# Optimization experiments

Hardware: AMD Instinct MI355X
Metric: run time of the kernel (lower is better)

The kernel has to match this reference:

```python
import jax, jax.numpy as jnp
import numpy as np

B, C, H, W = 2, 512, 48, 48
HEADS, DHEAD = 8, 64
INNER = HEADS * DHEAD  # 512
CTX_LEN, CTX_DIM = 77, 768
FF_INNER = 4 * INNER   # 2048 (GEGLU inner dim)
GN_GROUPS, GN_EPS, LN_EPS = 32, 1e-6, 1e-5
SCALE = DHEAD ** -0.5


def setup_inputs() -> dict:
    key = jax.random.key(0)
    ks = iter(jax.random.split(key, 32))
    def nrm(shape, s=0.02):
        return jax.random.normal(next(ks), shape, jnp.float32) * s
    return dict(
        x=jax.random.normal(next(ks), (B, C, H, W), jnp.float32),
        context=jax.random.normal(next(ks), (B, CTX_LEN, CTX_DIM), jnp.float32),
        gn_g=jnp.ones((C,), jnp.float32), gn_b=jnp.zeros((C,), jnp.float32),
        w_in=nrm((C, INNER)), b_in=jnp.zeros((INNER,), jnp.float32),
        ln1_g=jnp.ones((INNER,), jnp.float32), ln1_b=jnp.zeros((INNER,), jnp.float32),
        wq1=nrm((INNER, INNER)), wk1=nrm((INNER, INNER)), wv1=nrm((INNER, INNER)),
        wo1=nrm((INNER, INNER)), bo1=jnp.zeros((INNER,), jnp.float32),
        ln2_g=jnp.ones((INNER,), jnp.float32), ln2_b=jnp.zeros((INNER,), jnp.float32),
        wq2=nrm((INNER, INNER)), wk2=nrm((CTX_DIM, INNER)), wv2=nrm((CTX_DIM, INNER)),
        wo2=nrm((INNER, INNER)), bo2=jnp.zeros((INNER,), jnp.float32),
        ln3_g=jnp.ones((INNER,), jnp.float32), ln3_b=jnp.zeros((INNER,), jnp.float32),
        w_ff1=nrm((INNER, 2 * FF_INNER)), b_ff1=jnp.zeros((2 * FF_INNER,), jnp.float32),
        w_ff2=nrm((FF_INNER, INNER)), b_ff2=jnp.zeros((INNER,), jnp.float32),
        w_out=nrm((INNER, C)), b_out=jnp.zeros((C,), jnp.float32),
    )


def _layernorm(x, g, b):
    m = jnp.mean(x, -1, keepdims=True)
    v = jnp.var(x, -1, keepdims=True)
    return (x - m) * jax.lax.rsqrt(v + LN_EPS) * g + b


def _groupnorm(x, g, b):
    bs, c, h, w = x.shape
    xg = x.reshape(bs, GN_GROUPS, c // GN_GROUPS, h, w)
    m = jnp.mean(xg, (2, 3, 4), keepdims=True)
    v = jnp.var(xg, (2, 3, 4), keepdims=True)
    xg = (xg - m) * jax.lax.rsqrt(v + GN_EPS)
    return xg.reshape(bs, c, h, w) * g[None, :, None, None] + b[None, :, None, None]


def _attn(x, ctx, wq, wk, wv, wo, bo):
    bs, n, _ = x.shape
    m = ctx.shape[1]
    q = (x @ wq).reshape(bs, n, HEADS, DHEAD).transpose(0, 2, 1, 3)    # b h n d
    k = (ctx @ wk).reshape(bs, m, HEADS, DHEAD).transpose(0, 2, 1, 3)  # b h m d
    v = (ctx @ wv).reshape(bs, m, HEADS, DHEAD).transpose(0, 2, 1, 3)
    sim = jnp.einsum('bhid,bhjd->bhij', q, k) * SCALE
    a = jax.nn.softmax(sim, axis=-1)
    o = jnp.einsum('bhij,bhjd->bhid', a, v)
    o = o.transpose(0, 2, 1, 3).reshape(bs, n, INNER)
    return o @ wo + bo


def reference(x, context, gn_g, gn_b, w_in, b_in,
              ln1_g, ln1_b, wq1, wk1, wv1, wo1, bo1,
              ln2_g, ln2_b, wq2, wk2, wv2, wo2, bo2,
              ln3_g, ln3_b, w_ff1, b_ff1, w_ff2, b_ff2,
              w_out, b_out):
    x_in = x
    h = _groupnorm(x, gn_g, gn_b)
    # proj_in: 1x1 conv == channel-wise linear
    h = jnp.einsum('bchw,cd->bdhw', h, w_in) + b_in[None, :, None, None]
    t = h.reshape(B, INNER, H * W).transpose(0, 2, 1)  # b n c
    # BasicTransformerBlock (depth=1)
    hn = _layernorm(t, ln1_g, ln1_b)
    t = _attn(hn, hn, wq1, wk1, wv1, wo1, bo1) + t          # self-attention
    hn = _layernorm(t, ln2_g, ln2_b)
    t = _attn(hn, context, wq2, wk2, wv2, wo2, bo2) + t     # cross-attention
    hn = _layernorm(t, ln3_g, ln3_b)
    u = hn @ w_ff1 + b_ff1                                   # GEGLU proj
    a_, g_ = jnp.split(u, 2, axis=-1)
    t = (a_ * jax.nn.gelu(g_, approximate=False)) @ w_ff2 + b_ff2 + t
    # back to image + proj_out 1x1 conv + residual
    y = t.transpose(0, 2, 1).reshape(B, INNER, H, W)
    y = jnp.einsum('bchw,cd->bdhw', y, w_out) + b_out[None, :, None, None]
    return y + x_in
```

## Files before the change

kernel.cpp:

```cpp
#include <hip/hip_runtime.h>
#include <hip/hip_bf16.h>

typedef __bf16 bf16_t;
typedef __bf16 bf16x4 __attribute__((ext_vector_type(4)));
typedef __bf16 bf16x8 __attribute__((ext_vector_type(8)));
typedef float f32x4 __attribute__((ext_vector_type(4)));

static __device__ __forceinline__ bf16x8 bzero8() {
  bf16x8 v;
#pragma unroll
  for (int j = 0; j < 8; j++) v[j] = (bf16_t)0.f;
  return v;
}

static __device__ __forceinline__ void async_copy16(const bf16_t* g, bf16_t* l) {
  __builtin_amdgcn_global_load_lds((const __attribute__((address_space(1))) void*)g,
                                   (__attribute__((address_space(3))) void*)l,
                                   16, 0, 0);
}
#define WAVE_LGKM() asm volatile("s_waitcnt lgkmcnt(0)" ::: "memory")

static __device__ __forceinline__ float fast_exp2(float x) {
  float r;
  asm volatile("v_exp_f32 %0, %1" : "=v"(r) : "v"(x));
  return r;
}

#define QK_SCALE 0.18033688f

__global__ void probe_kernel(const void* x, int* flag) {
  if (threadIdx.x != 0 || blockIdx.x != 0) return;
  const unsigned short* u = (const unsigned short*)x;
  int insane = 0;
  for (int j = 0; j < 512; j++) {
    unsigned short h = u[j];
    int e = (h >> 7) & 0xFF;
    if (e == 0xFF || e > 140 || (e != 0 && e < 100)) insane++;
  }
  *flag = (insane > 16) ? 1 : 0;
}

struct ConvArgs { const void* src[28]; int n[28]; int off[28]; };
__global__ __launch_bounds__(256) void convert_kernel(ConvArgs a, const int* flag,
                                                      bf16_t* dst) {
  int i = blockIdx.y;
  if (i >= 28) return;
  int n = a.n[i];
  if (n == 0) return;
  const void* s = a.src[i];
  bf16_t* d = dst + a.off[i];
  bool f32 = (*flag != 0);
  int n4 = n >> 2;
  for (int j = blockIdx.x * 256 + threadIdx.x; j < n4; j += gridDim.x * 256) {
    bf16x4 o;
    if (f32) {
      float4 v = ((const float4*)s)[j];
      o[0] = (bf16_t)v.x; o[1] = (bf16_t)v.y; o[2] = (bf16_t)v.z; o[3] = (bf16_t)v.w;
    } else {
      o = ((const bf16x4*)s)[j];
    }
    ((bf16x4*)d)[j] = o;
  }
  int base = n4 << 2;
  int j = base + blockIdx.x * 256 + threadIdx.x;
  if (j < n) {
    float v = f32 ? ((const float*)s)[j] : (float)((const bf16_t*)s)[j];
    d[j] = (bf16_t)v;
  }
}

struct TransArgs { const void* src[10]; int dst_off[10]; int K[10]; int N[10]; };
__global__ __launch_bounds__(256) void transpose_kernel(TransArgs ta, const int* flag,
                                                        bf16_t* __restrict__ wt) {
  int wi = blockIdx.y;
  int K = ta.K[wi], N = ta.N[wi];
  int tiles_n = N >> 6;
  int tile = blockIdx.x;
  if (tile >= tiles_n * (K >> 6)) return;
  int tk = tile / tiles_n, tn = tile - tk * tiles_n;
  int k0 = tk * 64, n0 = tn * 64;
  bf16_t* dst = wt + ta.dst_off[wi];
  bool f32 = (*flag != 0);
  __shared__ bf16_t tl[64][66];
  int t = threadIdx.x;
  int r = t >> 2, c = (t & 3) * 16;
  if (f32) {
    const float* src = (const float*)ta.src[wi] + (size_t)(k0 + r) * N + n0 + c;
#pragma unroll
    for (int q = 0; q < 4; q++) {
      float4 v = *(const float4*)(src + q * 4);
      tl[r][c + q * 4 + 0] = (bf16_t)v.x;
      tl[r][c + q * 4 + 1] = (bf16_t)v.y;
      tl[r][c + q * 4 + 2] = (bf16_t)v.z;
      tl[r][c + q * 4 + 3] = (bf16_t)v.w;
    }
  } else {
    const bf16_t* src = (const bf16_t*)ta.src[wi] + (size_t)(k0 + r) * N + n0 + c;
    bf16x8 v0 = *(const bf16x8*)(src);
    bf16x8 v1 = *(const bf16x8*)(src + 8);
#pragma unroll
    for (int j = 0; j < 8; j++) { tl[r][c + j] = v0[j]; tl[r][c + 8 + j] = v1[j]; }
  }
  __syncthreads();
  bf16x8 o0, o1;
#pragma unroll
  for (int j = 0; j < 8; j++) { o0[j] = tl[c + j][r]; o1[j] = tl[c + 8 + j][r]; }
  *(bf16x8*)(dst + (size_t)(n0 + r) * K + k0 + c) = o0;
  *(bf16x8*)(dst + (size_t)(n0 + r) * K + k0 + c + 8) = o1;
}

__global__ __launch_bounds__(256) void gn_stats_kernel(const bf16_t* __restrict__ x,
                                                       float* __restrict__ stats) {
  const bf16x8* base = (const bf16x8*)(x + (size_t)blockIdx.x * 36864);
  float s = 0.f, ss = 0.f;
  for (int i = threadIdx.x; i < 4608; i += 256) {
    bf16x8 v = base[i];
#pragma unroll
    for (int j = 0; j < 8; j++) { float f = (float)v[j]; s += f; ss += f * f; }
  }
  __shared__ float red[8];
#pragma unroll
  for (int off = 32; off > 0; off >>= 1) { s += __shfl_down(s, off); ss += __shfl_down(ss, off); }
  int wid = threadIdx.x >> 6;
  if ((threadIdx.x & 63) == 0) { red[wid] = s; red[4 + wid] = ss; }
  __syncthreads();
  if (threadIdx.x == 0) {
    float S = red[0] + red[1] + red[2] + red[3];
    float SS = red[4] + red[5] + red[6] + red[7];
    const float inv = 1.0f / 36864.0f;
    float mean = S * inv;
    float var = SS * inv - mean * mean;
    stats[blockIdx.x * 2] = mean;
    stats[blockIdx.x * 2 + 1] = rsqrtf(fmaxf(var, 0.f) + 1e-6f);
  }
}

__global__ __launch_bounds__(256) void gn_apply_kernel(const bf16_t* __restrict__ x,
                                                       const float* __restrict__ stats,
                                                       const bf16_t* __restrict__ g,
                                                       const bf16_t* __restrict__ bb,
                                                       bf16_t* __restrict__ xnt) {
  int p0 = blockIdx.x * 64, c0 = blockIdx.y * 64, bz = blockIdx.z;
  __shared__ bf16_t tl[64][66];
  int t = threadIdx.x;
  int r = t >> 2, cc = (t & 3) * 16;
  int c = c0 + r;
  float mean = stats[(bz * 32 + (c >> 4)) * 2];
  float rstd = stats[(bz * 32 + (c >> 4)) * 2 + 1];
  float gg = (float)g[c], bbv = (float)bb[c];
  const bf16_t* row = x + ((size_t)(bz * 512 + c)) * 2304 + p0 + cc;
  bf16x8 v0 = *(const bf16x8*)(row);
  bf16x8 v1 = *(const bf16x8*)(row + 8);
#pragma unroll
  for (int j = 0; j < 8; j++) {
    tl[r][cc + j] = (bf16_t)(((float)v0[j] - mean) * rstd * gg + bbv);
    tl[r][cc + 8 + j] = (bf16_t)(((float)v1[j] - mean) * rstd * gg + bbv);
  }
  __syncthreads();
  bf16x8 o0, o1;
#pragma unroll
  for (int j = 0; j < 8; j++) { o0[j] = tl[cc + j][r]; o1[j] = tl[cc + 8 + j][r]; }
  bf16_t* orow = xnt + ((size_t)(bz * 2304 + p0 + r)) * 512 + c0 + cc;
  *(bf16x8*)(orow) = o0;
  *(bf16x8*)(orow + 8) = o1;
}

__global__ __launch_bounds__(256) void ln_kernel(const float* __restrict__ in,
                                                 const bf16_t* __restrict__ g,
                                                 const bf16_t* __restrict__ b,
                                                 bf16_t* __restrict__ out) {
  int tok = blockIdx.x * 4 + (threadIdx.x >> 6);
  int lane = threadIdx.x & 63;
  const float* row = in + (size_t)tok * 512 + lane * 8;
  float f[8];
  float s = 0.f, ss = 0.f;
#pragma unroll
  for (int j = 0; j < 8; j++) { f[j] = row[j]; s += f[j]; ss += f[j] * f[j]; }
#pragma unroll
  for (int off = 32; off > 0; off >>= 1) { s += __shfl_xor(s, off); ss += __shfl_xor(ss, off); }
  float mean = s * (1.0f / 512.0f);
  float var = ss * (1.0f / 512.0f) - mean * mean;
  float rstd = rsqrtf(fmaxf(var, 0.f) + 1e-5f);
  bf16x8 gv = *(const bf16x8*)(g + lane * 8);
  bf16x8 bv = *(const bf16x8*)(b + lane * 8);
  bf16x8 o;
#pragma unroll
  for (int j = 0; j < 8; j++) o[j] = (bf16_t)((f[j] - mean) * rstd * (float)gv[j] + (float)bv[j]);
  *(bf16x8*)(out + (size_t)tok * 512 + lane * 8) = o;
}

template <int SMODE, int MODE>
__global__ __launch_bounds__(256) void gemm64d_kernel(
    const bf16_t* __restrict__ A, int lda,
    const bf16_t* __restrict__ Bt, int K, int N,
    const bf16_t* __restrict__ bias, float oscale,
    float* __restrict__ t32, bf16_t* __restrict__ C,
    const bf16_t* __restrict__ resb, const float* __restrict__ resf,
    float* __restrict__ Cf, const int* dflag) {
  __shared__ bf16_t As[2][4096];
  __shared__ bf16_t Bs[2][4096];
  int t = threadIdx.x, w = t >> 6, quad = (t >> 4) & 3, l16 = t & 15;
  int m0 = blockIdx.y * 64, n0 = blockIdx.x * 64;
  int wm = (w >> 1) * 32, wn = (w & 1) * 32;
  const f32x4 z4 = {0.f, 0.f, 0.f, 0.f};
  f32x4 acc[2][2] = {{z4, z4}, {z4, z4}};
  int r0 = t >> 3, c0 = ((t & 7) ^ (r0 & 7)) * 8;
  int r1 = r0 + 32, c1 = ((t & 7) ^ (r1 & 7)) * 8;
  const bf16_t* Ar0 = A + (size_t)(m0 + r0) * lda + c0;
  const bf16_t* Ar1 = A + (size_t)(m0 + r1) * lda + c1;
  const bf16_t* Br0 = Bt + (size_t)(n0 + r0) * K + c0;
  const bf16_t* Br1 = Bt + (size_t)(n0 + r1) * K + c1;
  int niter = K >> 6;
  async_copy16(Ar0, As[0] + w * 512);
  async_copy16(Ar1, As[0] + 2048 + w * 512);
  async_copy16(Br0, Bs[0] + w * 512);
  async_copy16(Br1, Bs[0] + 2048 + w * 512);
  for (int it = 0; it < niter; it++) {
    __syncthreads();
    if (it + 1 < niter) {
      int k0 = (it + 1) << 6;
      int nb = (it + 1) & 1;
      async_copy16(Ar0 + k0, As[nb] + w * 512);
      async_copy16(Ar1 + k0, As[nb] + 2048 + w * 512);
      async_copy16(Br0 + k0, Bs[nb] + w * 512);
      async_copy16(Br1 + k0, Bs[nb] + 2048 + w * 512);
    }
    int cb = it & 1;
    bf16x8 af[2][2], bff[2][2];
#pragma unroll
    for (int mi = 0; mi < 2; mi++) {
      int rr = wm + mi * 16 + l16;
      af[mi][0] = *(const bf16x8*)&As[cb][(rr * 8 + (quad ^ (rr & 7))) * 8];
      af[mi][1] = *(const bf16x8*)&As[cb][(rr * 8 + ((quad + 4) ^ (rr & 7))) * 8];
    }
#pragma unroll
    for (int ni = 0; ni < 2; ni++) {
      int rr = wn + ni * 16 + l16;
      bff[ni][0] = *(const bf16x8*)&Bs[cb][(rr * 8 + (quad ^ (rr & 7))) * 8];
      bff[ni][1] = *(const bf16x8*)&Bs[cb][(rr * 8 + ((quad + 4) ^ (rr & 7))) * 8];
    }
#pragma unroll
    for (int mi = 0; mi < 2; mi++)
#pragma unroll
      for (int ni = 0; ni < 2; ni++) {
        acc[mi][ni] = __builtin_amdgcn_mfma_f32_16x16x32_bf16(af[mi][0], bff[ni][0], acc[mi][ni], 0, 0, 0);
        acc[mi][ni] = __builtin_amdgcn_mfma_f32_16x16x32_bf16(af[mi][1], bff[ni][1], acc[mi][ni], 0, 0, 0);
      }
  }
  const bool f32m = (MODE == 3) && (*dflag != 0);
#pragma unroll
  for (int mi = 0; mi < 2; mi++)
#pragma unroll
    for (int ni = 0; ni < 2; ni++) {
      int col = n0 + wn + ni * 16 + l16;
      float bv = bias ? (float)bias[col] : 0.f;
#pragma unroll
      for (int r = 0; r < 4; r++) {
        int row = m0 + wm + mi * 16 + quad * 4 + r;
        float v = acc[mi][ni][r] + bv;
        size_t addr;
        if (SMODE == 0) {
          addr = (size_t)row * N + col;
        } else {
          int b2 = row / 2304; int p = row - b2 * 2304;
          addr = ((size_t)(b2 * 512 + col)) * 2304 + p;
        }
        if (MODE == 0) C[addr] = (bf16_t)(v * oscale);
        else if (MODE == 1) { t32[addr] = v; C[addr] = (bf16_t)v; }
        else if (MODE == 2) { v += t32[addr]; t32[addr] = v; C[addr] = (bf16_t)v; }
        else {
          v += f32m ? resf[addr] : (float)resb[addr];
          if (f32m) Cf[addr] = v; else C[addr] = (bf16_t)v;
        }
      }
    }
}

__global__ __launch_bounds__(256) void qkv_kernel(
    const bf16_t* __restrict__ A,
    const bf16_t* __restrict__ BtQ, const bf16_t* __restrict__ BtK,
    const bf16_t* __restrict__ BtV,
    bf16_t* __restrict__ Qo, bf16_t* __restrict__ Ko, bf16_t* __restrict__ Vt) {
  __shared__ bf16_t As[2][4096];
  __shared__ bf16_t Bs[2][4096];
  int z = blockIdx.z;
  const bf16_t* Bt = (z == 0) ? BtQ : (z == 1) ? BtK : BtV;
  int t = threadIdx.x, w = t >> 6, quad = (t >> 4) & 3, l16 = t & 15;
  int m0 = blockIdx.y * 64, n0 = blockIdx.x * 64;
  int wm = (w >> 1) * 32, wn = (w & 1) * 32;
  const f32x4 z4 = {0.f, 0.f, 0.f, 0.f};
  f32x4 acc[2][2] = {{z4, z4}, {z4, z4}};
  int r0 = t >> 3, c0 = ((t & 7) ^ (r0 & 7)) * 8;
  int r1 = r0 + 32, c1 = ((t & 7) ^ (r1 & 7)) * 8;
  const bf16_t* Ar0 = A + (size_t)(m0 + r0) * 512 + c0;
  const bf16_t* Ar1 = A + (size_t)(m0 + r1) * 512 + c1;
  const bf16_t* Br0 = Bt + (size_t)(n0 + r0) * 512 + c0;
  const bf16_t* Br1 = Bt + (size_t)(n0 + r1) * 512 + c1;
  async_copy16(Ar0, As[0] + w * 512);
  async_copy16(Ar1, As[0] + 2048 + w * 512);
  async_copy16(Br0, Bs[0] + w * 512);
  async_copy16(Br1, Bs[0] + 2048 + w * 512);
  for (int it = 0; it < 8; it++) {
    __syncthreads();
    if (it + 1 < 8) {
      int k0 = (it + 1) << 6;
      int nb = (it + 1) & 1;
      async_copy16(Ar0 + k0, As[nb] + w * 512);
      async_copy16(Ar1 + k0, As[nb] + 2048 + w * 512);
      async_copy16(Br0 + k0, Bs[nb] + w * 512);
      async_copy16(Br1 + k0, Bs[nb] + 2048 + w * 512);
    }
    int cb = it & 1;
    bf16x8 af[2][2], bff[2][2];
#pragma unroll
    for (int mi = 0; mi < 2; mi++) {
      int rr = wm + mi * 16 + l16;
      af[mi][0] = *(const bf16x8*)&As[cb][(rr * 8 + (quad ^ (rr & 7))) * 8];
      af[mi][1] = *(const bf16x8*)&As[cb][(rr * 8 + ((quad + 4) ^ (rr & 7))) * 8];
    }
#pragma unroll
    for (int ni = 0; ni < 2; ni++) {
      int rr = wn + ni * 16 + l16;
      bff[ni][0] = *(const bf16x8*)&Bs[cb][(rr * 8 + (quad ^ (rr & 7))) * 8];
      bff[ni][1] = *(const bf16x8*)&Bs[cb][(rr * 8 + ((quad + 4) ^ (rr & 7))) * 8];
    }
#pragma unroll
    for (int mi = 0; mi < 2; mi++)
#pragma unroll
      for (int ni = 0; ni < 2; ni++) {
        acc[mi][ni] = __builtin_amdgcn_mfma_f32_16x16x32_bf16(af[mi][0], bff[ni][0], acc[mi][ni], 0, 0, 0);
        acc[mi][ni] = __builtin_amdgcn_mfma_f32_16x16x32_bf16(af[mi][1], bff[ni][1], acc[mi][ni], 0, 0, 0);
      }
  }
#pragma unroll
  for (int mi = 0; mi < 2; mi++)
#pragma unroll
    for (int ni = 0; ni < 2; ni++) {
      int col = n0 + wn + ni * 16 + l16;
#pragma unroll
      for (int r = 0; r < 4; r++) {
        int row = m0 + wm + mi * 16 + quad * 4 + r;
        float v = acc[mi][ni][r];
        if (z == 0) Qo[(size_t)row * 512 + col] = (bf16_t)(v * QK_SCALE);
        else if (z == 1) Ko[(size_t)row * 512 + col] = (bf16_t)v;
        else {
          int b2 = row / 2304; int p = row - b2 * 2304;
          Vt[((size_t)(b2 * 512 + col)) * 2304 + p] = (bf16_t)v;
        }
      }
    }
}

__global__ __launch_bounds__(256) void ff1_kernel(const bf16_t* __restrict__ A,
                                                  const bf16_t* __restrict__ Bt,
                                                  const bf16_t* __restrict__ bias,
                                                  bf16_t* __restrict__ U) {
  __shared__ bf16_t As[2][4096];
  __shared__ bf16_t Ba[2][4096];
  __shared__ bf16_t Bg[2][4096];
  int t = threadIdx.x, w = t >> 6, quad = (t >> 4) & 3, l16 = t & 15;
  int m0 = blockIdx.y * 64, n0 = blockIdx.x * 64;
  int wm = (w >> 1) * 32, wn = (w & 1) * 32;
  const f32x4 z4 = {0.f, 0.f, 0.f, 0.f};
  f32x4 aa[2][2] = {{z4, z4}, {z4, z4}};
  f32x4 ag[2][2] = {{z4, z4}, {z4, z4}};
  int r0 = t >> 3, c0 = ((t & 7) ^ (r0 & 7)) * 8;
  int r1 = r0 + 32, c1 = ((t & 7) ^ (r1 & 7)) * 8;
  const bf16_t* Ar0 = A + (size_t)(m0 + r0) * 512 + c0;
  const bf16_t* Ar1 = A + (size_t)(m0 + r1) * 512 + c1;
  const bf16_t* Ba0 = Bt + (size_t)(n0 + r0) * 512 + c0;
  const bf16_t* Ba1 = Bt + (size_t)(n0 + r1) * 512 + c1;
  const bf16_t* Bg0 = Bt + (size_t)(2048 + n0 + r0) * 512 + c0;
  const bf16_t* Bg1 = Bt + (size_t)(2048 + n0 + r1) * 512 + c1;
  async_copy16(Ar0, As[0] + w * 512);
  async_copy16(Ar1, As[0] + 2048 + w * 512);
  async_copy16(Ba0, Ba[0] + w * 512);
  async_copy16(Ba1, Ba[0] + 2048 + w * 512);
  async_copy16(Bg0, Bg[0] + w * 512);
  async_copy16(Bg1, Bg[0] + 2048 + w * 512);
  for (int it = 0; it < 8; it++) {
    __syncthreads();
    if (it + 1 < 8) {
      int k0 = (it + 1) << 6;
      int nb = (it + 1) & 1;
      async_copy16(Ar0 + k0, As[nb] + w * 512);
      async_copy16(Ar1 + k0, As[nb] + 2048 + w * 512);
      async_copy16(Ba0 + k0, Ba[nb] + w * 512);
      async_copy16(Ba1 + k0, Ba[nb] + 2048 + w * 512);
      async_copy16(Bg0 + k0, Bg[nb] + w * 512);
      async_copy16(Bg1 + k0, Bg[nb] + 2048 + w * 512);
    }
    int cb = it & 1;
    bf16x8 af[2][2], ba[2][2], bg[2][2];
#pragma unroll
    for (int mi = 0; mi < 2; mi++) {
      int rr = wm + mi * 16 + l16;
      af[mi][0] = *(const bf16x8*)&As[cb][(rr * 8 + (quad ^ (rr & 7))) * 8];
      af[mi][1] = *(const bf16x8*)&As[cb][(rr * 8 + ((quad + 4) ^ (rr & 7))) * 8];
    }
#pragma unroll
    for (int ni = 0; ni < 2; ni++) {
      int rr = wn + ni * 16 + l16;
      int o0 = (rr * 8 + (quad ^ (rr & 7))) * 8;
      int o1 = (rr * 8 + ((quad + 4) ^ (rr & 7))) * 8;
      ba[ni][0] = *(const bf16x8*)&Ba[cb][o0];
      ba[ni][1] = *(const bf16x8*)&Ba[cb][o1];
      bg[ni][0] = *(const bf16x8*)&Bg[cb][o0];
      bg[ni][1] = *(const bf16x8*)&Bg[cb][o1];
    }
#pragma unroll
    for (int mi = 0; mi < 2; mi++)
#pragma unroll
      for (int ni = 0; ni < 2; ni++) {
        aa[mi][ni] = __builtin_amdgcn_mfma_f32_16x16x32_bf16(af[mi][0], ba[ni][0], aa[mi][ni], 0, 0, 0);
        aa[mi][ni] = __builtin_amdgcn_mfma_f32_16x16x32_bf16(af[mi][1], ba[ni][1], aa[mi][ni], 0, 0, 0);
        ag[mi][ni] = __builtin_amdgcn_mfma_f32_16x16x32_bf16(af[mi][0], bg[ni][0], ag[mi][ni], 0, 0, 0);
        ag[mi][ni] = __builtin_amdgcn_mfma_f32_16x16x32_bf16(af[mi][1], bg[ni][1], ag[mi][ni], 0, 0, 0);
      }
  }
#pragma unroll
  for (int mi = 0; mi < 2; mi++)
#pragma unroll
    for (int ni = 0; ni < 2; ni++) {
      int col = n0 + wn + ni * 16 + l16;
      float bba = (float)bias[col], bbg = (float)bias[col + 2048];
#pragma unroll
      for (int r = 0; r < 4; r++) {
        int row = m0 + wm + mi * 16 + quad * 4 + r;
        float a = aa[mi][ni][r] + bba;
        float g = ag[mi][ni][r] + bbg;
        float gl = 0.5f * g * (1.0f + erff(g * 0.70710678118654752f));
        U[(size_t)row * 2048 + col] = (bf16_t)(a * gl);
      }
    }
}

template <int SMODE>
__global__ __launch_bounds__(256) void gemm64s_kernel(const bf16_t* __restrict__ A,
                                                      const bf16_t* __restrict__ B,
                                                      bf16_t* __restrict__ C,
                                                      int M, int N, int K, int lda) {
  __shared__ alignas(16) bf16_t As[64][40];
  __shared__ alignas(16) bf16_t Bs[64][40];
  int t = threadIdx.x;
  int m0 = blockIdx.y * 64, n0 = blockIdx.x * 64;
  int w = t >> 6, lane = t & 63, quad = lane >> 4, l16 = lane & 15;
  int ar = t >> 2, ac = (t & 3) * 8;
  int br = t >> 3, bc = (t & 7) * 8;
  const f32x4 z4 = {0.f, 0.f, 0.f, 0.f};
  f32x4 acc[4] = {z4, z4, z4, z4};
  int gm = m0 + ar;
  const bool a_ok = gm < M;
  for (int k0 = 0; k0 < K; k0 += 32) {
    bf16x8 av = a_ok ? *(const bf16x8*)(A + (size_t)gm * lda + k0 + ac) : bzero8();
    bf16x8 bv = *(const bf16x8*)(B + (size_t)(k0 + br) * N + n0 + bc);
    __syncthreads();
    *(bf16x8*)(&As[ar][ac]) = av;
#pragma unroll
    for (int j = 0; j < 8; j++) Bs[bc + j][br] = bv[j];
    __syncthreads();
    bf16x8 afrag = *(const bf16x8*)(&As[w * 16 + l16][quad * 8]);
#pragma unroll
    for (int kb = 0; kb < 4; kb++) {
      bf16x8 bfrag = *(const bf16x8*)(&Bs[kb * 16 + l16][quad * 8]);
      acc[kb] = __builtin_amdgcn_mfma_f32_16x16x32_bf16(afrag, bfrag, acc[kb], 0, 0, 0);
    }
  }
#pragma unroll
  for (int kb = 0; kb < 4; kb++) {
    int col = n0 + kb * 16 + l16;
#pragma unroll
    for (int r = 0; r < 4; r++) {
      int row = m0 + w * 16 + quad * 4 + r;
      if (row < M) {
        float v = acc[kb][r];
        size_t addr;
        if (SMODE == 0) addr = (size_t)row * N + col;
        else { int b2 = row / 77; int p = row - b2 * 77; addr = ((size_t)(b2 * 512 + col)) * 128 + p; }
        C[addr] = (bf16_t)v;
      }
    }
  }
}

template <bool MASK>
__global__ __launch_bounds__(256) void flash5_kernel(const bf16_t* __restrict__ q,
                                                     const bf16_t* __restrict__ kk,
                                                     const bf16_t* __restrict__ vt,
                                                     bf16_t* __restrict__ out,
                                                     int n_k, int kv_bstride, int vt_len) {
  __shared__ bf16_t Ks[2][4096];
  __shared__ bf16_t Vs[2][4096];
  __shared__ bf16_t p_lds[4][16 * 72];
  int t = threadIdx.x, w = t >> 6, quad = (t >> 4) & 3, l16 = t & 15;
  int b = blockIdx.y >> 3, h = blockIdx.y & 7;
  int q0 = blockIdx.x * 64 + w * 16;
  const bf16_t* qrow = q + ((size_t)(b * 2304 + q0 + l16)) * 512 + h * 64 + quad * 8;
  bf16x8 qa0 = *(const bf16x8*)(qrow);
  bf16x8 qa1 = *(const bf16x8*)(qrow + 32);
  const f32x4 z4 = {0.f, 0.f, 0.f, 0.f};
  f32x4 o[4] = {z4, z4, z4, z4};
  float l_i = 0.f;
  const bf16_t* kbase = kk + (size_t)b * kv_bstride + h * 64;
  const bf16_t* vbase = vt + ((size_t)((b * 8 + h) * 64)) * vt_len;
  int kr0 = t >> 3, kc0g = ((t & 7) ^ (kr0 & 7)) * 8;
  int kr1 = kr0 + 32, kc1g = ((t & 7) ^ (kr1 & 7)) * 8;
  int n_kt = (n_k + 63) >> 6;
  async_copy16(kbase + (size_t)kr0 * 512 + kc0g, Ks[0] + w * 512);
  async_copy16(kbase + (size_t)kr1 * 512 + kc1g, Ks[0] + 2048 + w * 512);
  async_copy16(vbase + (size_t)kr0 * vt_len + kc0g, Vs[0] + w * 512);
  async_copy16(vbase + (size_t)kr1 * vt_len + kc1g, Vs[0] + 2048 + w * 512);
  for (int kt = 0; kt < n_kt; kt++) {
    int kc0 = kt * 64;
    __syncthreads();
    if (kt + 1 < n_kt) {
      int kn = (kt + 1) * 64;
      int nb = (kt + 1) & 1;
      async_copy16(kbase + (size_t)(kn + kr0) * 512 + kc0g, Ks[nb] + w * 512);
      async_copy16(kbase + (size_t)(kn + kr1) * 512 + kc1g, Ks[nb] + 2048 + w * 512);
      async_copy16(vbase + (size_t)kr0 * vt_len + kn + kc0g, Vs[nb] + w * 512);
      async_copy16(vbase + (size_t)kr1 * vt_len + kn + kc1g, Vs[nb] + 2048 + w * 512);
    }
    int cb = kt & 1;
    bf16x8 kf[4][2], vf[4][2];
#pragma unroll
    for (int kb = 0; kb < 4; kb++) {
      int rr = kb * 16 + l16;
#pragma unroll
      for (int c = 0; c < 2; c++) {
        int gi = (rr * 8 + ((quad + c * 4) ^ (rr & 7))) * 8;
        kf[kb][c] = *(const bf16x8*)&Ks[cb][gi];
        vf[kb][c] = *(const bf16x8*)&Vs[cb][gi];
      }
    }
    f32x4 s[4] = {z4, z4, z4, z4};
#pragma unroll
    for (int kb = 0; kb < 4; kb++) {
      s[kb] = __builtin_amdgcn_mfma_f32_16x16x32_bf16(kf[kb][0], qa0, s[kb], 0, 0, 0);
      s[kb] = __builtin_amdgcn_mfma_f32_16x16x32_bf16(kf[kb][1], qa1, s[kb], 0, 0, 0);
    }
    float rs = 0.f;
#pragma unroll
    for (int kb = 0; kb < 4; kb++)
#pragma unroll
      for (int r = 0; r < 4; r++) {
        float sv = s[kb][r];
        if (MASK && (kc0 + kb * 16 + quad * 4 + r) >= n_k) sv = -1e30f;
        float pp = fast_exp2(sv);
        s[kb][r] = pp;
        rs += pp;
      }
    rs += __shfl_xor(rs, 16);
    rs += __shfl_xor(rs, 32);
    l_i += rs;
    WAVE_LGKM();
#pragma unroll
    for (int kb = 0; kb < 4; kb++) {
      bf16x4 pk;
#pragma unroll
      for (int r = 0; r < 4; r++) pk[r] = (bf16_t)s[kb][r];
      *(bf16x4*)&p_lds[w][l16 * 72 + kb * 16 + quad * 4] = pk;
    }
    WAVE_LGKM();
    bf16x8 pa0 = *(const bf16x8*)&p_lds[w][l16 * 72 + quad * 8];
    bf16x8 pa1 = *(const bf16x8*)&p_lds[w][l16 * 72 + 32 + quad * 8];
#pragma unroll
    for (int db = 0; db < 4; db++) {
      o[db] = __builtin_amdgcn_mfma_f32_16x16x32_bf16(vf[db][0], pa0, o[db], 0, 0, 0);
      o[db] = __builtin_amdgcn_mfma_f32_16x16x32_bf16(vf[db][1], pa1, o[db], 0, 0, 0);
    }
  }
  float inv = 1.0f / l_i;
  bf16_t* orow = out + ((size_t)(b * 2304 + q0 + l16)) * 512 + h * 64 + quad * 4;
#pragma unroll
  for (int db = 0; db < 4; db++) {
    bf16x4 pk;
#pragma unroll
    for (int r = 0; r < 4; r++) pk[r] = (bf16_t)(o[db][r] * inv);
    *(bf16x4*)(orow + db * 16) = pk;
  }
}

extern "C" void kernel_launch(void* const* d_in, const int* in_sizes, int n_in,
                              void* d_out, int out_size, void* d_ws, size_t ws_size,
                              hipStream_t stream) {
  (void)out_size; (void)ws_size;
  char* p = (char*)d_ws;
  int* flag = (int*)p;
  float* stats = (float*)(p + 16);
  float* t32 = (float*)(p + 1024);
  const size_t TOK512 = (size_t)4608 * 512;
  bf16_t* conv = (bf16_t*)(p + 1024 + TOK512 * 4);

  const int widx[10] = {4, 8, 9, 10, 11, 15, 18, 22, 24, 26};
  const int wK[10] = {512, 512, 512, 512, 512, 512, 512, 512, 2048, 512};
  const int wN[10] = {512, 512, 512, 512, 512, 512, 512, 4096, 512, 512};
  bool is_wt[28] = {};
  for (int i = 0; i < 10; i++) is_wt[widx[i]] = true;

  ConvArgs ca;
  int off = 0;
  int noff[28];
  for (int i = 0; i < 28; i++) {
    ca.src[i] = (i < n_in) ? d_in[i] : nullptr;
    ca.n[i] = (i < n_in && !is_wt[i]) ? in_sizes[i] : 0;
    ca.off[i] = off;
    noff[i] = off;
    int sz = (i < n_in) ? in_sizes[i] : 0;
    off += ((is_wt[i] ? 0 : sz) + 7) & ~7;
  }
  bf16_t* wt = conv + ((off + 7) & ~7);
  TransArgs ta;
  int woff = 0, wtoff[10];
  for (int i = 0; i < 10; i++) {
    ta.src[i] = d_in[widx[i]];
    ta.dst_off[i] = woff;
    wtoff[i] = woff;
    ta.K[i] = wK[i]; ta.N[i] = wN[i];
    woff += wK[i] * wN[i];
  }
  bf16_t* hn  = wt + woff;
  bf16_t* tb  = hn + TOK512;
  bf16_t* xnt = tb + TOK512;
  bf16_t* qb  = xnt + TOK512;
  bf16_t* kbuf = qb + TOK512;
  bf16_t* vtb = kbuf + TOK512;
  bf16_t* ub2 = xnt;
  bf16_t* ob  = xnt;

  const bf16_t* xb    = conv + noff[0];
  const bf16_t* ctxb  = conv + noff[1];
  const bf16_t* gn_g  = conv + noff[2];
  const bf16_t* gn_b  = conv + noff[3];
  const bf16_t* b_in  = conv + noff[5];
  const bf16_t* ln1_g = conv + noff[6];
  const bf16_t* ln1_b = conv + noff[7];
  const bf16_t* bo1   = conv + noff[12];
  const bf16_t* ln2_g = conv + noff[13];
  const bf16_t* ln2_b = conv + noff[14];
  const bf16_t* wk2   = conv + noff[16];
  const bf16_t* wv2   = conv + noff[17];
  const bf16_t* bo2   = conv + noff[19];
  const bf16_t* ln3_g = conv + noff[20];
  const bf16_t* ln3_b = conv + noff[21];
  const bf16_t* b_ff1 = conv + noff[23];
  const bf16_t* b_ff2 = conv + noff[25];
  const bf16_t* b_out = conv + noff[27];
  const bf16_t* wt_in  = wt + wtoff[0];
  const bf16_t* wt_q1  = wt + wtoff[1];
  const bf16_t* wt_k1  = wt + wtoff[2];
  const bf16_t* wt_v1  = wt + wtoff[3];
  const bf16_t* wt_o1  = wt + wtoff[4];
  const bf16_t* wt_q2  = wt + wtoff[5];
  const bf16_t* wt_o2  = wt + wtoff[6];
  const bf16_t* wt_ff1 = wt + wtoff[7];
  const bf16_t* wt_ff2 = wt + wtoff[8];
  const bf16_t* wt_out = wt + wtoff[9];

  probe_kernel<<<1, 64, 0, stream>>>(d_in[0], flag);
  convert_kernel<<<dim3(128, 28), 256, 0, stream>>>(ca, flag, conv);
  transpose_kernel<<<dim3(512, 10), 256, 0, stream>>>(ta, flag, wt);

  gn_stats_kernel<<<64, 256, 0, stream>>>(xb, stats);
  gn_apply_kernel<<<dim3(36, 8, 2), 256, 0, stream>>>(xb, stats, gn_g, gn_b, xnt);
  gemm64d_kernel<0, 1><<<dim3(8, 72), 256, 0, stream>>>(xnt, 512, wt_in, 512, 512, b_in, 1.f, t32, tb, nullptr, nullptr, nullptr, nullptr);
  ln_kernel<<<1152, 256, 0, stream>>>(t32, ln1_g, ln1_b, hn);
  qkv_kernel<<<dim3(8, 72, 3), 256, 0, stream>>>(hn, wt_q1, wt_k1, wt_v1, qb, kbuf, vtb);
  flash5_kernel<false><<<dim3(36, 16), 256, 0, stream>>>(qb, kbuf, vtb, ob, 2304, 2304 * 512, 2304);
  gemm64d_kernel<0, 2><<<dim3(8, 72), 256, 0, stream>>>(ob, 512, wt_o1, 512, 512, bo1, 1.f, t32, tb, nullptr, nullptr, nullptr, nullptr);
  ln_kernel<<<1152, 256, 0, stream>>>(t32, ln2_g, ln2_b, hn);
  gemm64d_kernel<0, 0><<<dim3(8, 72), 256, 0, stream>>>(hn, 512, wt_q2, 512, 512, nullptr, QK_SCALE, nullptr, qb, nullptr, nullptr, nullptr, nullptr);
  gemm64s_kernel<0><<<dim3(8, 3), 256, 0, stream>>>(ctxb, wk2, kbuf, 154, 512, 768, 768);
  gemm64s_kernel<2><<<dim3(8, 3), 256, 0, stream>>>(ctxb, wv2, vtb, 154, 512, 768, 768);
  flash5_kernel<true><<<dim3(36, 16), 256, 0, stream>>>(qb, kbuf, vtb, ob, 77, 77 * 512, 128);
  gemm64d_kernel<0, 2><<<dim3(8, 72), 256, 0, stream>>>(ob, 512, wt_o2, 512, 512, bo2, 1.f, t32, tb, nullptr, nullptr, nullptr, nullptr);
  ln_kernel<<<1152, 256, 0, stream>>>(t32, ln3_g, ln3_b, hn);
  ff1_kernel<<<dim3(32, 72), 256, 0, stream>>>(hn, wt_ff1, b_ff1, ub2);
  gemm64d_kernel<0, 2><<<dim3(8, 72), 256, 0, stream>>>(ub2, 2048, wt_ff2, 2048, 512, b_ff2, 1.f, t32, tb, nullptr, nullptr, nullptr, nullptr);
  gemm64d_kernel<1, 3><<<dim3(8, 72), 256, 0, stream>>>(tb, 512, wt_out, 512, 512, b_out, 1.f, nullptr, (bf16_t*)d_out, xb, (const float*)d_in[0], (float*)d_out, flag);
}
```

Before: 424.2 us.

## Load GEMM weights directly to registers, merge cross-attn KV GEMMs, widen flash query tile

The GEMM kernels (gemm64d, qkv, ff1) stop staging the B (weight) tile through LDS and instead load each wave's B fragments straight from global memory into registers, prefetched one k-step ahead. This cuts LDS traffic and LDS footprint, but each block now reads more weight bytes from global/L2 with narrower per-lane accesses. The two cross-attention K/V projection launches are merged into one kernel using blockIdx.z. The flash attention kernel now runs 128-thread blocks where each wave handles 32 query rows, reusing each K/V fragment loaded from LDS for two query sub-tiles, at the cost of more registers and fewer waves per block.

```diff
diff --git a/kernel.cpp b/kernel.cpp
--- a/kernel.cpp
+++ b/kernel.cpp
@@ -198,7 +198,6 @@
     const bf16_t* __restrict__ resb, const float* __restrict__ resf,
     float* __restrict__ Cf, const int* dflag) {
   __shared__ bf16_t As[2][4096];
-  __shared__ bf16_t Bs[2][4096];
   int t = threadIdx.x, w = t >> 6, quad = (t >> 4) & 3, l16 = t & 15;
   int m0 = blockIdx.y * 64, n0 = blockIdx.x * 64;
   int wm = (w >> 1) * 32, wn = (w & 1) * 32;
@@ -208,13 +207,18 @@
   int r1 = r0 + 32, c1 = ((t & 7) ^ (r1 & 7)) * 8;
   const bf16_t* Ar0 = A + (size_t)(m0 + r0) * lda + c0;
   const bf16_t* Ar1 = A + (size_t)(m0 + r1) * lda + c1;
-  const bf16_t* Br0 = Bt + (size_t)(n0 + r0) * K + c0;
-  const bf16_t* Br1 = Bt + (size_t)(n0 + r1) * K + c1;
+  const bf16_t* Brow[2];
+  Brow[0] = Bt + (size_t)(n0 + wn + l16) * K;
+  Brow[1] = Bt + (size_t)(n0 + wn + 16 + l16) * K;
   int niter = K >> 6;
+  bf16x8 bcur[2][2], bnxt[2][2];
+#pragma unroll
+  for (int ni = 0; ni < 2; ni++)
+#pragma unroll
+    for (int c = 0; c < 2; c++)
+      bcur[ni][c] = *(const bf16x8*)(Brow[ni] + (quad + c * 4) * 8);
   async_copy16(Ar0, As[0] + w * 512);
   async_copy16(Ar1, As[0] + 2048 + w * 512);
-  async_copy16(Br0, Bs[0] + w * 512);
-  async_copy16(Br1, Bs[0] + 2048 + w * 512);
   for (int it = 0; it < niter; it++) {
     __syncthreads();
     if (it + 1 < niter) {
@@ -222,11 +226,14 @@
       int nb = (it + 1) & 1;
       async_copy16(Ar0 + k0, As[nb] + w * 512);
       async_copy16(Ar1 + k0, As[nb] + 2048 + w * 512);
-      async_copy16(Br0 + k0, Bs[nb] + w * 512);
-      async_copy16(Br1 + k0, Bs[nb] + 2048 + w * 512);
+#pragma unroll
+      for (int ni = 0; ni < 2; ni++)
+#pragma unroll
+        for (int c = 0; c < 2; c++)
+          bnxt[ni][c] = *(const bf16x8*)(Brow[ni] + k0 + (quad + c * 4) * 8);
     }
     int cb = it & 1;
-    bf16x8 af[2][2], bff[2][2];
+    bf16x8 af[2][2];
 #pragma unroll
     for (int mi = 0; mi < 2; mi++) {
       int rr = wm + mi * 16 + l16;
@@ -234,18 +241,18 @@
       af[mi][1] = *(const bf16x8*)&As[cb][(rr * 8 + ((quad + 4) ^ (rr & 7))) * 8];
     }
 #pragma unroll
-    for (int ni = 0; ni < 2; ni++) {
-      int rr = wn + ni * 16 + l16;
-      bff[ni][0] = *(const bf16x8*)&Bs[cb][(rr * 8 + (quad ^ (rr & 7))) * 8];
-      bff[ni][1] = *(const bf16x8*)&Bs[cb][(rr * 8 + ((quad + 4) ^ (rr & 7))) * 8];
-    }
-#pragma unroll
     for (int mi = 0; mi < 2; mi++)
 #pragma unroll
       for (int ni = 0; ni < 2; ni++) {
-        acc[mi][ni] = __builtin_amdgcn_mfma_f32_16x16x32_bf16(af[mi][0], bff[ni][0], acc[mi][ni], 0, 0, 0);
-        acc[mi][ni] = __builtin_amdgcn_mfma_f32_16x16x32_bf16(af[mi][1], bff[ni][1], acc[mi][ni], 0, 0, 0);
-      }
+        acc[mi][ni] = __builtin_amdgcn_mfma_f32_16x16x32_bf16(af[mi][0], bcur[ni][0], acc[mi][ni], 0, 0, 0);
+        acc[mi][ni] = __builtin_amdgcn_mfma_f32_16x16x32_bf16(af[mi][1], bcur[ni][1], acc[mi][ni], 0, 0, 0);
+      }
+    if (it + 1 < niter) {
+#pragma unroll
+      for (int ni = 0; ni < 2; ni++)
+#pragma unroll
+        for (int c = 0; c < 2; c++) bcur[ni][c] = bnxt[ni][c];
+    }
   }
   const bool f32m = (MODE == 3) && (*dflag != 0);
 #pragma unroll
@@ -282,7 +289,6 @@
     const bf16_t* __restrict__ BtV,
     bf16_t* __restrict__ Qo, bf16_t* __restrict__ Ko, bf16_t* __restrict__ Vt) {
   __shared__ bf16_t As[2][4096];
-  __shared__ bf16_t Bs[2][4096];
   int z = blockIdx.z;
   const bf16_t* Bt = (z == 0) ? BtQ : (z == 1) ? BtK : BtV;
   int t = threadIdx.x, w = t >> 6, quad = (t >> 4) & 3, l16 = t & 15;
@@ -294,12 +300,17 @@
   int r1 = r0 + 32, c1 = ((t & 7) ^ (r1 & 7)) * 8;
   const bf16_t* Ar0 = A + (size_t)(m0 + r0) * 512 + c0;
   const bf16_t* Ar1 = A + (size_t)(m0 + r1) * 512 + c1;
-  const bf16_t* Br0 = Bt + (size_t)(n0 + r0) * 512 + c0;
-  const bf16_t* Br1 = Bt + (size_t)(n0 + r1) * 512 + c1;
+  const bf16_t* Brow[2];
+  Brow[0] = Bt + (size_t)(n0 + wn + l16) * 512;
+  Brow[1] = Bt + (size_t)(n0 + wn + 16 + l16) * 512;
+  bf16x8 bcur[2][2], bnxt[2][2];
+#pragma unroll
+  for (int ni = 0; ni < 2; ni++)
+#pragma unroll
+    for (int c = 0; c < 2; c++)
+      bcur[ni][c] = *(const bf16x8*)(Brow[ni] + (quad + c * 4) * 8);
   async_copy16(Ar0, As[0] + w * 512);
   async_copy16(Ar1, As[0] + 2048 + w * 512);
-  async_copy16(Br0, Bs[0] + w * 512);
-  async_copy16(Br1, Bs[0] + 2048 + w * 512);
   for (int it = 0; it < 8; it++) {
     __syncthreads();
     if (it + 1 < 8) {
@@ -307,11 +318,14 @@
       int nb = (it + 1) & 1;
       async_copy16(Ar0 + k0, As[nb] + w * 512);
       async_copy16(Ar1 + k0, As[nb] + 2048 + w * 512);
-      async_copy16(Br0 + k0, Bs[nb] + w * 512);
-      async_copy16(Br1 + k0, Bs[nb] + 2048 + w * 512);
+#pragma unroll
+      for (int ni = 0; ni < 2; ni++)
+#pragma unroll
+        for (int c = 0; c < 2; c++)
+          bnxt[ni][c] = *(const bf16x8*)(Brow[ni] + k0 + (quad + c * 4) * 8);
     }
     int cb = it & 1;
-    bf16x8 af[2][2], bff[2][2];
+    bf16x8 af[2][2];
 #pragma unroll
     for (int mi = 0; mi < 2; mi++) {
       int rr = wm + mi * 16 + l16;
@@ -319,18 +333,18 @@
       af[mi][1] = *(const bf16x8*)&As[cb][(rr * 8 + ((quad + 4) ^ (rr & 7))) * 8];
     }
 #pragma unroll
-    for (int ni = 0; ni < 2; ni++) {
-      int rr = wn + ni * 16 + l16;
-      bff[ni][0] = *(const bf16x8*)&Bs[cb][(rr * 8 + (quad ^ (rr & 7))) * 8];
-      bff[ni][1] = *(const bf16x8*)&Bs[cb][(rr * 8 + ((quad + 4) ^ (rr & 7))) * 8];
-    }
-#pragma unroll
     for (int mi = 0; mi < 2; mi++)
 #pragma unroll
       for (int ni = 0; ni < 2; ni++) {
-        acc[mi][ni] = __builtin_amdgcn_mfma_f32_16x16x32_bf16(af[mi][0], bff[ni][0], acc[mi][ni], 0, 0, 0);
-        acc[mi][ni] = __builtin_amdgcn_mfma_f32_16x16x32_bf16(af[mi][1], bff[ni][1], acc[mi][ni], 0, 0, 0);
-      }
+        acc[mi][ni] = __builtin_amdgcn_mfma_f32_16x16x32_bf16(af[mi][0], bcur[ni][0], acc[mi][ni], 0, 0, 0);
+        acc[mi][ni] = __builtin_amdgcn_mfma_f32_16x16x32_bf16(af[mi][1], bcur[ni][1], acc[mi][ni], 0, 0, 0);
+      }
+    if (it + 1 < 8) {
+#pragma unroll
+      for (int ni = 0; ni < 2; ni++)
+#pragma unroll
+        for (int c = 0; c < 2; c++) bcur[ni][c] = bnxt[ni][c];
+    }
   }
 #pragma unroll
   for (int mi = 0; mi < 2; mi++)
@@ -356,8 +370,6 @@
                                                   const bf16_t* __restrict__ bias,
                                                   bf16_t* __restrict__ U) {
   __shared__ bf16_t As[2][4096];
-  __shared__ bf16_t Ba[2][4096];
-  __shared__ bf16_t Bg[2][4096];
   int t = threadIdx.x, w = t >> 6, quad = (t >> 4) & 3, l16 = t & 15;
   int m0 = blockIdx.y * 64, n0 = blockIdx.x * 64;
   int wm = (w >> 1) * 32, wn = (w & 1) * 32;
@@ -368,16 +380,22 @@
   int r1 = r0 + 32, c1 = ((t & 7) ^ (r1 & 7)) * 8;
   const bf16_t* Ar0 = A + (size_t)(m0 + r0) * 512 + c0;
   const bf16_t* Ar1 = A + (size_t)(m0 + r1) * 512 + c1;
-  const bf16_t* Ba0 = Bt + (size_t)(n0 + r0) * 512 + c0;
-  const bf16_t* Ba1 = Bt + (size_t)(n0 + r1) * 512 + c1;
-  const bf16_t* Bg0 = Bt + (size_t)(2048 + n0 + r0) * 512 + c0;
-  const bf16_t* Bg1 = Bt + (size_t)(2048 + n0 + r1) * 512 + c1;
+  const bf16_t* BrA[2];
+  const bf16_t* BrG[2];
+  BrA[0] = Bt + (size_t)(n0 + wn + l16) * 512;
+  BrA[1] = Bt + (size_t)(n0 + wn + 16 + l16) * 512;
+  BrG[0] = Bt + (size_t)(2048 + n0 + wn + l16) * 512;
+  BrG[1] = Bt + (size_t)(2048 + n0 + wn + 16 + l16) * 512;
+  bf16x8 bca[2][2], bna[2][2], bcg[2][2], bng[2][2];
+#pragma unroll
+  for (int ni = 0; ni < 2; ni++)
+#pragma unroll
+    for (int c = 0; c < 2; c++) {
+      bca[ni][c] = *(const bf16x8*)(BrA[ni] + (quad + c * 4) * 8);
+      bcg[ni][c] = *(const bf16x8*)(BrG[ni] + (quad + c * 4) * 8);
+    }
   async_copy16(Ar0, As[0] + w * 512);
   async_copy16(Ar1, As[0] + 2048 + w * 512);
-  async_copy16(Ba0, Ba[0] + w * 512);
-  async_copy16(Ba1, Ba[0] + 2048 + w * 512);
-  async_copy16(Bg0, Bg[0] + w * 512);
-  async_copy16(Bg1, Bg[0] + 2048 + w * 512);
   for (int it = 0; it < 8; it++) {
     __syncthreads();
     if (it + 1 < 8) {
@@ -385,13 +403,16 @@
       int nb = (it + 1) & 1;
       async_copy16(Ar0 + k0, As[nb] + w * 512);
       async_copy16(Ar1 + k0, As[nb] + 2048 + w * 512);
-      async_copy16(Ba0 + k0, Ba[nb] + w * 512);
-      async_copy16(Ba1 + k0, Ba[nb] + 2048 + w * 512);
-      async_copy16(Bg0 + k0, Bg[nb] + w * 512);
-      async_copy16(Bg1 + k0, Bg[nb] + 2048 + w * 512);
+#pragma unroll
+      for (int ni = 0; ni < 2; ni++)
+#pragma unroll
+        for (int c = 0; c < 2; c++) {
+          bna[ni][c] = *(const bf16x8*)(BrA[ni] + k0 + (quad + c * 4) * 8);
+          bng[ni][c] = *(const bf16x8*)(BrG[ni] + k0 + (quad + c * 4) * 8);
+        }
     }
     int cb = it & 1;
-    bf16x8 af[2][2], ba[2][2], bg[2][2];
+    bf16x8 af[2][2];
 #pragma unroll
     for (int mi = 0; mi < 2; mi++) {
       int rr = wm + mi * 16 + l16;
@@ -399,24 +420,20 @@
       af[mi][1] = *(const bf16x8*)&As[cb][(rr * 8 + ((quad + 4) ^ (rr & 7))) * 8];
     }
 #pragma unroll
-    for (int ni = 0; ni < 2; ni++) {
-      int rr = wn + ni * 16 + l16;
-      int o0 = (rr * 8 + (quad ^ (rr & 7))) * 8;
-      int o1 = (rr * 8 + ((quad + 4) ^ (rr & 7))) * 8;
-      ba[ni][0] = *(const bf16x8*)&Ba[cb][o0];
-      ba[ni][1] = *(const bf16x8*)&Ba[cb][o1];
-      bg[ni][0] = *(const bf16x8*)&Bg[cb][o0];
-      bg[ni][1] = *(const bf16x8*)&Bg[cb][o1];
-    }
-#pragma unroll
     for (int mi = 0; mi < 2; mi++)
 #pragma unroll
       for (int ni = 0; ni < 2; ni++) {
-        aa[mi][ni] = __builtin_amdgcn_mfma_f32_16x16x32_bf16(af[mi][0], ba[ni][0], aa[mi][ni], 0, 0, 0);
-        aa[mi][ni] = __builtin_amdgcn_mfma_f32_16x16x32_bf16(af[mi][1], ba[ni][1], aa[mi][ni], 0, 0, 0);
-        ag[mi][ni] = __builtin_amdgcn_mfma_f32_16x16x32_bf16(af[mi][0], bg[ni][0], ag[mi][ni], 0, 0, 0);
-        ag[mi][ni] = __builtin_amdgcn_mfma_f32_16x16x32_bf16(af[mi][1], bg[ni][1], ag[mi][ni], 0, 0, 0);
-      }
+        aa[mi][ni] = __builtin_amdgcn_mfma_f32_16x16x32_bf16(af[mi][0], bca[ni][0], aa[mi][ni], 0, 0, 0);
+        aa[mi][ni] = __builtin_amdgcn_mfma_f32_16x16x32_bf16(af[mi][1], bca[ni][1], aa[mi][ni], 0, 0, 0);
+        ag[mi][ni] = __builtin_amdgcn_mfma_f32_16x16x32_bf16(af[mi][0], bcg[ni][0], ag[mi][ni], 0, 0, 0);
+        ag[mi][ni] = __builtin_amdgcn_mfma_f32_16x16x32_bf16(af[mi][1], bcg[ni][1], ag[mi][ni], 0, 0, 0);
+      }
+    if (it + 1 < 8) {
+#pragma unroll
+      for (int ni = 0; ni < 2; ni++)
+#pragma unroll
+        for (int c = 0; c < 2; c++) { bca[ni][c] = bna[ni][c]; bcg[ni][c] = bng[ni][c]; }
+    }
   }
 #pragma unroll
   for (int mi = 0; mi < 2; mi++)
@@ -435,11 +452,14 @@
     }
 }
 
-template <int SMODE>
-__global__ __launch_bounds__(256) void gemm64s_kernel(const bf16_t* __restrict__ A,
-                                                      const bf16_t* __restrict__ B,
-                                                      bf16_t* __restrict__ C,
-                                                      int M, int N, int K, int lda) {
+__global__ __launch_bounds__(256) void kv2_kernel(const bf16_t* __restrict__ A,
+                                                  const bf16_t* __restrict__ Bk,
+                                                  const bf16_t* __restrict__ Bv,
+                                                  bf16_t* __restrict__ Ck,
+                                                  bf16_t* __restrict__ Cv) {
+  const int M = 154, N = 512, K = 768;
+  int z = blockIdx.z;
+  const bf16_t* B = z ? Bv : Bk;
   __shared__ alignas(16) bf16_t As[64][40];
   __shared__ alignas(16) bf16_t Bs[64][40];
   int t = threadIdx.x;
@@ -452,7 +472,7 @@
   int gm = m0 + ar;
   const bool a_ok = gm < M;
   for (int k0 = 0; k0 < K; k0 += 32) {
-    bf16x8 av = a_ok ? *(const bf16x8*)(A + (size_t)gm * lda + k0 + ac) : bzero8();
+    bf16x8 av = a_ok ? *(const bf16x8*)(A + (size_t)gm * K + k0 + ac) : bzero8();
     bf16x8 bv = *(const bf16x8*)(B + (size_t)(k0 + br) * N + n0 + bc);
     __syncthreads();
     *(bf16x8*)(&As[ar][ac]) = av;
@@ -474,52 +494,68 @@
       int row = m0 + w * 16 + quad * 4 + r;
       if (row < M) {
         float v = acc[kb][r];
-        size_t addr;
-        if (SMODE == 0) addr = (size_t)row * N + col;
-        else { int b2 = row / 77; int p = row - b2 * 77; addr = ((size_t)(b2 * 512 + col)) * 128 + p; }
-        C[addr] = (bf16_t)v;
+        if (z == 0) Ck[(size_t)row * N + col] = (bf16_t)v;
+        else {
+          int b2 = row / 77; int p = row - b2 * 77;
+          Cv[((size_t)(b2 * 512 + col)) * 128 + p] = (bf16_t)v;
+        }
       }
     }
   }
 }
 
 template <bool MASK>
-__global__ __launch_bounds__(256) void flash5_kernel(const bf16_t* __restrict__ q,
+__global__ __launch_bounds__(128) void flash6_kernel(const bf16_t* __restrict__ q,
                                                      const bf16_t* __restrict__ kk,
                                                      const bf16_t* __restrict__ vt,
                                                      bf16_t* __restrict__ out,
                                                      int n_k, int kv_bstride, int vt_len) {
   __shared__ bf16_t Ks[2][4096];
   __shared__ bf16_t Vs[2][4096];
-  __shared__ bf16_t p_lds[4][16 * 72];
+  __shared__ bf16_t p_lds[2][32 * 72];
   int t = threadIdx.x, w = t >> 6, quad = (t >> 4) & 3, l16 = t & 15;
   int b = blockIdx.y >> 3, h = blockIdx.y & 7;
-  int q0 = blockIdx.x * 64 + w * 16;
-  const bf16_t* qrow = q + ((size_t)(b * 2304 + q0 + l16)) * 512 + h * 64 + quad * 8;
-  bf16x8 qa0 = *(const bf16x8*)(qrow);
-  bf16x8 qa1 = *(const bf16x8*)(qrow + 32);
+  int q0 = blockIdx.x * 64 + w * 32;
+  bf16x8 qa[2][2];
+#pragma unroll
+  for (int si = 0; si < 2; si++) {
+    const bf16_t* qrow = q + ((size_t)(b * 2304 + q0 + si * 16 + l16)) * 512 + h * 64 + quad * 8;
+    qa[si][0] = *(const bf16x8*)(qrow);
+    qa[si][1] = *(const bf16x8*)(qrow + 32);
+  }
   const f32x4 z4 = {0.f, 0.f, 0.f, 0.f};
-  f32x4 o[4] = {z4, z4, z4, z4};
-  float l_i = 0.f;
+  f32x4 o[2][4];
+  float l_i[2] = {0.f, 0.f};
+#pragma unroll
+  for (int si = 0; si < 2; si++)
+#pragma unroll
+    for (int db = 0; db < 4; db++) o[si][db] = z4;
   const bf16_t* kbase = kk + (size_t)b * kv_bstride + h * 64;
   const bf16_t* vbase = vt + ((size_t)((b * 8 + h) * 64)) * vt_len;
-  int kr0 = t >> 3, kc0g = ((t & 7) ^ (kr0 & 7)) * 8;
-  int kr1 = kr0 + 32, kc1g = ((t & 7) ^ (kr1 & 7)) * 8;
+  int kr[4], kc[4];
+#pragma unroll
+  for (int i = 0; i < 4; i++) {
+    int g = t + 128 * i;
+    kr[i] = g >> 3;
+    kc[i] = ((g & 7) ^ (kr[i] & 7)) * 8;
+  }
   int n_kt = (n_k + 63) >> 6;
-  async_copy16(kbase + (size_t)kr0 * 512 + kc0g, Ks[0] + w * 512);
-  async_copy16(kbase + (size_t)kr1 * 512 + kc1g, Ks[0] + 2048 + w * 512);
-  async_copy16(vbase + (size_t)kr0 * vt_len + kc0g, Vs[0] + w * 512);
-  async_copy16(vbase + (size_t)kr1 * vt_len + kc1g, Vs[0] + 2048 + w * 512);
+#pragma unroll
+  for (int i = 0; i < 4; i++) {
+    async_copy16(kbase + (size_t)kr[i] * 512 + kc[i], Ks[0] + w * 512 + i * 1024);
+    async_copy16(vbase + (size_t)kr[i] * vt_len + kc[i], Vs[0] + w * 512 + i * 1024);
+  }
   for (int kt = 0; kt < n_kt; kt++) {
     int kc0 = kt * 64;
     __syncthreads();
     if (kt + 1 < n_kt) {
       int kn = (kt + 1) * 64;
       int nb = (kt + 1) & 1;
-      async_copy16(kbase + (size_t)(kn + kr0) * 512 + kc0g, Ks[nb] + w * 512);
-      async_copy16(kbase + (size_t)(kn + kr1) * 512 + kc1g, Ks[nb] + 2048 + w * 512);
-      async_copy16(vbase + (size_t)kr0 * vt_len + kn + kc0g, Vs[nb] + w * 512);
-      async_copy16(vbase + (size_t)kr1 * vt_len + kn + kc1g, Vs[nb] + 2048 + w * 512);
+#pragma unroll
+      for (int i = 0; i < 4; i++) {
+        async_copy16(kbase + (size_t)(kn + kr[i]) * 512 + kc[i], Ks[nb] + w * 512 + i * 1024);
+        async_copy16(vbase + (size_t)kr[i] * vt_len + kn + kc[i], Vs[nb] + w * 512 + i * 1024);
+      }
     }
     int cb = kt & 1;
     bf16x8 kf[4][2], vf[4][2];
@@ -533,51 +569,57 @@
         vf[kb][c] = *(const bf16x8*)&Vs[cb][gi];
       }
     }
-    f32x4 s[4] = {z4, z4, z4, z4};
-#pragma unroll
-    for (int kb = 0; kb < 4; kb++) {
-      s[kb] = __builtin_amdgcn_mfma_f32_16x16x32_bf16(kf[kb][0], qa0, s[kb], 0, 0, 0);
-      s[kb] = __builtin_amdgcn_mfma_f32_16x16x32_bf16(kf[kb][1], qa1, s[kb], 0, 0, 0);
-    }
-    float rs = 0.f;
-#pragma unroll
-    for (int kb = 0; kb < 4; kb++)
-#pragma unroll
-      for (int r = 0; r < 4; r++) {
-        float sv = s[kb][r];
-        if (MASK && (kc0 + kb * 16 + quad * 4 + r) >= n_k) sv = -1e30f;
-        float pp = fast_exp2(sv);
-        s[kb][r] = pp;
-        rs += pp;
-      }
-    rs += __shfl_xor(rs, 16);
-    rs += __shfl_xor(rs, 32);
-    l_i += rs;
-    WAVE_LGKM();
-#pragma unroll
-    for (int kb = 0; kb < 4; kb++) {
+#pragma unroll
+    for (int si = 0; si < 2; si++) {
+      f32x4 s[4] = {z4, z4, z4, z4};
+#pragma unroll
+      for (int kb = 0; kb < 4; kb++) {
+        s[kb] = __builtin_amdgcn_mfma_f32_16x16x32_bf16(kf[kb][0], qa[si][0], s[kb], 0, 0, 0);
+        s[kb] = __builtin_amdgcn_mfma_f32_16x16x32_bf16(kf[kb][1], qa[si][1], s[kb], 0, 0, 0);
+      }
+      float rs = 0.f;
+#pragma unroll
+      for (int kb = 0; kb < 4; kb++)
+#pragma unroll
+        for (int r = 0; r < 4; r++) {
+          float sv = s[kb][r];
+          if (MASK && (kc0 + kb * 16 + quad * 4 + r) >= n_k) sv = -1e30f;
+          float pp = fast_exp2(sv);
+          s[kb][r] = pp;
+          rs += pp;
+        }
+      rs += __shfl_xor(rs, 16);
+      rs += __shfl_xor(rs, 32);
+      l_i[si] += rs;
+      WAVE_LGKM();
+#pragma unroll
+      for (int kb = 0; kb < 4; kb++) {
+        bf16x4 pk;
+#pragma unroll
+        for (int r = 0; r < 4; r++) pk[r] = (bf16_t)s[kb][r];
+        *(bf16x4*)&p_lds[w][(si * 16 + l16) * 72 + kb * 16 + quad * 4] = pk;
+      }
+      WAVE_LGKM();
+      bf16x8 pa0 = *(const bf16x8*)&p_lds[w][(si * 16 + l16) * 72 + quad * 8];
+      bf16x8 pa1 = *(const bf16x8*)&p_lds[w][(si * 16 + l16) * 72 + 32 + quad * 8];
+#pragma unroll
+      for (int db = 0; db < 4; db++) {
+        o[si][db] = __builtin_amdgcn_mfma_f32_16x16x32_bf16(vf[db][0], pa0, o[si][db], 0, 0, 0);
+        o[si][db] = __builtin_amdgcn_mfma_f32_16x16x32_bf16(vf[db][1], pa1, o[si][db], 0, 0, 0);
+      }
+    }
+  }
+#pragma unroll
+  for (int si = 0; si < 2; si++) {
+    float inv = 1.0f / l_i[si];
+    bf16_t* orow = out + ((size_t)(b * 2304 + q0 + si * 16 + l16)) * 512 + h * 64 + quad * 4;
+#pragma unroll
+    for (int db = 0; db < 4; db++) {
       bf16x4 pk;
 #pragma unroll
-      for (int r = 0; r < 4; r++) pk[r] = (bf16_t)s[kb][r];
-      *(bf16x4*)&p_lds[w][l16 * 72 + kb * 16 + quad * 4] = pk;
-    }
-    WAVE_LGKM();
-    bf16x8 pa0 = *(const bf16x8*)&p_lds[w][l16 * 72 + quad * 8];
-    bf16x8 pa1 = *(const bf16x8*)&p_lds[w][l16 * 72 + 32 + quad * 8];
-#pragma unroll
-    for (int db = 0; db < 4; db++) {
-      o[db] = __builtin_amdgcn_mfma_f32_16x16x32_bf16(vf[db][0], pa0, o[db], 0, 0, 0);
-      o[db] = __builtin_amdgcn_mfma_f32_16x16x32_bf16(vf[db][1], pa1, o[db], 0, 0, 0);
-    }
-  }
-  float inv = 1.0f / l_i;
-  bf16_t* orow = out + ((size_t)(b * 2304 + q0 + l16)) * 512 + h * 64 + quad * 4;
-#pragma unroll
-  for (int db = 0; db < 4; db++) {
-    bf16x4 pk;
-#pragma unroll
-    for (int r = 0; r < 4; r++) pk[r] = (bf16_t)(o[db][r] * inv);
-    *(bf16x4*)(orow + db * 16) = pk;
+      for (int r = 0; r < 4; r++) pk[r] = (bf16_t)(o[si][db][r] * inv);
+      *(bf16x4*)(orow + db * 16) = pk;
+    }
   }
 }
 
@@ -666,13 +708,12 @@
   gemm64d_kernel<0, 1><<<dim3(8, 72), 256, 0, stream>>>(xnt, 512, wt_in, 512, 512, b_in, 1.f, t32, tb, nullptr, nullptr, nullptr, nullptr);
   ln_kernel<<<1152, 256, 0, stream>>>(t32, ln1_g, ln1_b, hn);
   qkv_kernel<<<dim3(8, 72, 3), 256, 0, stream>>>(hn, wt_q1, wt_k1, wt_v1, qb, kbuf, vtb);
-  flash5_kernel<false><<<dim3(36, 16), 256, 0, stream>>>(qb, kbuf, vtb, ob, 2304, 2304 * 512, 2304);
+  flash6_kernel<false><<<dim3(36, 16), 128, 0, stream>>>(qb, kbuf, vtb, ob, 2304, 2304 * 512, 2304);
   gemm64d_kernel<0, 2><<<dim3(8, 72), 256, 0, stream>>>(ob, 512, wt_o1, 512, 512, bo1, 1.f, t32, tb, nullptr, nullptr, nullptr, nullptr);
   ln_kernel<<<1152, 256, 0, stream>>>(t32, ln2_g, ln2_b, hn);
   gemm64d_kernel<0, 0><<<dim3(8, 72), 256, 0, stream>>>(hn, 512, wt_q2, 512, 512, nullptr, QK_SCALE, nullptr, qb, nullptr, nullptr, nullptr, nullptr);
-  gemm64s_kernel<0><<<dim3(8, 3), 256, 0, stream>>>(ctxb, wk2, kbuf, 154, 512, 768, 768);
-  gemm64s_kernel<2><<<dim3(8, 3), 256, 0, stream>>>(ctxb, wv2, vtb, 154, 512, 768, 768);
-  flash5_kernel<true><<<dim3(36, 16), 256, 0, stream>>>(qb, kbuf, vtb, ob, 77, 77 * 512, 128);
+  kv2_kernel<<<dim3(8, 3, 2), 256, 0, stream>>>(ctxb, wk2, wv2, kbuf, vtb);
+  flash6_kernel<true><<<dim3(36, 16), 128, 0, stream>>>(qb, kbuf, vtb, ob, 77, 77 * 512, 128);
   gemm64d_kernel<0, 2><<<dim3(8, 72), 256, 0, stream>>>(ob, 512, wt_o2, 512, 512, bo2, 1.f, t32, tb, nullptr, nullptr, nullptr, nullptr);
   ln_kernel<<<1152, 256, 0, stream>>>(t32, ln3_g, ln3_b, hn);
   ff1_kernel<<<dim3(32, 72), 256, 0, stream>>>(hn, wt_ff1, b_ff1, ub2);
```

Result: slower. 528.0 us (+24.5%).
